# Kernel tuning notes

Hardware: AMD Instinct MI355X
Metric: run time of the kernel (lower is better)

The kernel has to match this reference:

```python
import jax, jax.numpy as jnp
import numpy as np

N_NODES = 50000


def _gcn_conv(x, edge_index, W, b, n_nodes):
    # PyG GCNConv: add self loops, symmetric normalization, then
    # out[dst] = sum_{src->dst} norm * (x[src] @ W) + b
    src, dst = edge_index[0], edge_index[1]
    loop = jnp.arange(n_nodes, dtype=src.dtype)
    src = jnp.concatenate([src, loop])
    dst = jnp.concatenate([dst, loop])
    deg = jax.ops.segment_sum(jnp.ones_like(src, dtype=x.dtype), dst, num_segments=n_nodes)
    dinv = jnp.where(deg > 0, jax.lax.rsqrt(deg), 0.0)
    norm = dinv[src] * dinv[dst]                      # [E+N]
    h = x @ W                                         # [N, out] dense GEMM first (in >= out here)
    msg = h[src] * norm[:, None]                      # gather + scale
    out = jax.ops.segment_sum(msg, dst, num_segments=n_nodes)  # scatter-add
    return out + b


def setup_inputs() -> dict:
    key = jax.random.key(0)
    k = jax.random.split(key, 5)
    in_c, hid_c, out_c = 128, 128, 64
    n, e = N_NODES, 800000
    x = jax.random.normal(k[0], (n, in_c), dtype=jnp.float32)
    edge_index = jax.random.randint(k[1], (2, e), 0, n, dtype=jnp.int64)
    # Glorot-ish scaled weights
    W1 = jax.random.normal(k[2], (in_c, hid_c), dtype=jnp.float32) * (1.0 / np.sqrt(in_c))
    b1 = jnp.zeros((hid_c,), dtype=jnp.float32)
    W2 = jax.random.normal(k[3], (hid_c, out_c), dtype=jnp.float32) * (1.0 / np.sqrt(hid_c))
    b2 = jnp.zeros((out_c,), dtype=jnp.float32)
    return {"x": x, "edge_index": edge_index, "W1": W1, "b1": b1, "W2": W2, "b2": b2}


def reference(x, edge_index, W1, b1, W2, b2):
    # Net.encode: conv1 -> relu -> conv2
    h = _gcn_conv(x, edge_index, W1, b1, N_NODES)
    h = jax.nn.relu(h)
    z = _gcn_conv(h, edge_index, W2, b2, N_NODES)
    return z
```

## Files before the change

kernel.cpp:

```cpp
#include <hip/hip_runtime.h>
#include <math.h>

constexpr int C_IN  = 128;
constexpr int C_HID = 128;
constexpr int C_OUT = 64;

typedef short bf8   __attribute__((ext_vector_type(8)));
typedef float f32x4 __attribute__((ext_vector_type(4)));

__device__ __forceinline__ int wave_incl_scan(int v, int lane) {
    #pragma unroll
    for (int off = 1; off < 64; off <<= 1) {
        int u = __shfl_up(v, off, 64);
        if (lane >= off) v += u;
    }
    return v;
}
__device__ __forceinline__ short b16(float f) {
    unsigned int u = __float_as_uint(f);
    u += 0x7FFFu + ((u >> 16) & 1u);
    return (short)(u >> 16);
}
__device__ __forceinline__ unsigned int bpack(float a, float b) {
    unsigned int ua = __float_as_uint(a), ub = __float_as_uint(b);
    ua += 0x7FFFu + ((ua >> 16) & 1u);
    ub += 0x7FFFu + ((ub >> 16) & 1u);
    return (ua >> 16) | (ub & 0xFFFF0000u);
}
__device__ __forceinline__ void acc8(float* a, const uint4 v) {
    a[0] += __uint_as_float(v.x << 16);
    a[1] += __uint_as_float(v.x & 0xFFFF0000u);
    a[2] += __uint_as_float(v.y << 16);
    a[3] += __uint_as_float(v.y & 0xFFFF0000u);
    a[4] += __uint_as_float(v.z << 16);
    a[5] += __uint_as_float(v.z & 0xFFFF0000u);
    a[6] += __uint_as_float(v.w << 16);
    a[7] += __uint_as_float(v.w & 0xFFFF0000u);
}

__global__ __launch_bounds__(256) void k_zero(int* __restrict__ p, int n4) {
    int i = blockIdx.x * 256 + threadIdx.x;
    if (i < n4) reinterpret_cast<int4*>(p)[i] = make_int4(0, 0, 0, 0);
}

__global__ __launch_bounds__(256) void k_count2(const int* __restrict__ dst, int e,
                                                int* __restrict__ cnt,
                                                int* __restrict__ slot) {
    int i = blockIdx.x * 256 + threadIdx.x;
    int base = i * 4;
    if (base >= e) return;
    if (base + 3 < e) {
        int4 d4 = *reinterpret_cast<const int4*>(dst + base);
        int4 s4;
        s4.x = atomicAdd(&cnt[d4.x], 1);
        s4.y = atomicAdd(&cnt[d4.y], 1);
        s4.z = atomicAdd(&cnt[d4.z], 1);
        s4.w = atomicAdd(&cnt[d4.w], 1);
        *reinterpret_cast<int4*>(slot + base) = s4;
    } else {
        for (int q = base; q < e; ++q) slot[q] = atomicAdd(&cnt[dst[q]], 1);
    }
}

__global__ __launch_bounds__(256) void k_scanAB(const int* __restrict__ cnt, int n,
                                                int* __restrict__ rowstart,
                                                int* __restrict__ blocksum,
                                                int* __restrict__ blockoff,
                                                int* __restrict__ ticket,
                                                float* __restrict__ dinv) {
    __shared__ int swave[4];
    __shared__ int amLast;
    const int tid = threadIdx.x, lane = tid & 63, w = tid >> 6;
    const int idx = blockIdx.x * 1024 + tid * 4;
    int4 c = make_int4(0, 0, 0, 0);
    if (idx + 3 < n) {
        c = *reinterpret_cast<const int4*>(cnt + idx);
    } else if (idx < n) {
        c.x = cnt[idx];
        if (idx + 1 < n) c.y = cnt[idx + 1];
        if (idx + 2 < n) c.z = cnt[idx + 2];
        if (idx + 3 < n) c.w = cnt[idx + 3];
    }
    if (idx + 0 < n) dinv[idx + 0] = rsqrtf((float)(c.x + 1));
    if (idx + 1 < n) dinv[idx + 1] = rsqrtf((float)(c.y + 1));
    if (idx + 2 < n) dinv[idx + 2] = rsqrtf((float)(c.z + 1));
    if (idx + 3 < n) dinv[idx + 3] = rsqrtf((float)(c.w + 1));

    const int s4 = c.x + c.y + c.z + c.w;
    const int incl = wave_incl_scan(s4, lane);
    if (lane == 63) swave[w] = incl;
    __syncthreads();
    int base = incl - s4;
    #pragma unroll
    for (int j = 0; j < 4; ++j) if (j < w) base += swave[j];

    if (idx + 3 < n) {
        int4 o;
        o.x = base;
        o.y = base + c.x;
        o.z = base + c.x + c.y;
        o.w = base + c.x + c.y + c.z;
        *reinterpret_cast<int4*>(rowstart + idx) = o;
    } else if (idx < n) {
        int acc = base;
        rowstart[idx] = acc; acc += c.x;
        if (idx + 1 < n) { rowstart[idx + 1] = acc; acc += c.y; }
        if (idx + 2 < n) { rowstart[idx + 2] = acc; acc += c.z; }
        if (idx + 3 < n) { rowstart[idx + 3] = acc; }
    }

    if (tid == 0) {
        int tot = swave[0] + swave[1] + swave[2] + swave[3];
        blocksum[blockIdx.x] = tot;
        if (blockIdx.x == gridDim.x - 1) rowstart[n] = tot;
        __threadfence();
        amLast = (atomicAdd(ticket, 1) == (int)gridDim.x - 1);
    }
    __syncthreads();
    if (amLast && tid < 64) {
        __threadfence();
        volatile int* bs = blocksum;
        const int nb = gridDim.x;
        int v = (tid < nb) ? bs[tid] : 0;
        int incl2 = wave_incl_scan(v, tid);
        if (tid < nb) blockoff[tid] = incl2 - v;
    }
}

__global__ __launch_bounds__(256) void k_fillgemm1(
    const int* __restrict__ src, const int* __restrict__ dst,
    const int* __restrict__ slot, int e, int nfb,
    const int* __restrict__ rowstart, const int* __restrict__ blockoff,
    unsigned short* __restrict__ nbr,
    const float* __restrict__ x, const float* __restrict__ W,
    const float* __restrict__ dinv, unsigned short* __restrict__ h1b, int n) {
    __shared__ short wf[8 * 4 * 64 * 8];
    if (blockIdx.x < nfb) {
        int i = blockIdx.x * 256 + threadIdx.x;
        int base = i * 4;
        if (base >= e) return;
        if (base + 3 < e) {
            int4 d4 = *reinterpret_cast<const int4*>(dst + base);
            int4 s4 = *reinterpret_cast<const int4*>(src + base);
            int4 t4 = *reinterpret_cast<const int4*>(slot + base);
            nbr[rowstart[d4.x] + blockoff[d4.x >> 10] + t4.x] = (unsigned short)s4.x;
            nbr[rowstart[d4.y] + blockoff[d4.y >> 10] + t4.y] = (unsigned short)s4.y;
            nbr[rowstart[d4.z] + blockoff[d4.z >> 10] + t4.z] = (unsigned short)s4.z;
            nbr[rowstart[d4.w] + blockoff[d4.w >> 10] + t4.w] = (unsigned short)s4.w;
        } else {
            for (int q = base; q < e; ++q) {
                int d = dst[q];
                nbr[rowstart[d] + blockoff[d >> 10] + slot[q]] = (unsigned short)src[q];
            }
        }
        return;
    }
    const int tid = threadIdx.x;
    for (int i = tid; i < 2048; i += 256) {
        const int l = i & 63, kt = (i >> 6) & 3, ct = i >> 8;
        const int krow = kt * 32 + ((l >> 4) << 3);
        const int col  = ct * 16 + (l & 15);
        const float* wp = W + (size_t)krow * C_HID + col;
        uint4 u;
        u.x = bpack(wp[0 * C_HID], wp[1 * C_HID]);
        u.y = bpack(wp[2 * C_HID], wp[3 * C_HID]);
        u.z = bpack(wp[4 * C_HID], wp[5 * C_HID]);
        u.w = bpack(wp[6 * C_HID], wp[7 * C_HID]);
        reinterpret_cast<uint4*>(wf)[i] = u;
    }
    __syncthreads();

    const int l = tid & 63, w = tid >> 6;
    const int row0 = (blockIdx.x - nfb) * 64 + w * 16;
    int arow = row0 + (l & 15);
    if (arow >= n) arow = n - 1;
    const float* xr = x + (size_t)arow * C_IN + ((l >> 4) << 3);

    bf8 a[4];
    #pragma unroll
    for (int kt = 0; kt < 4; ++kt) {
        float4 p0 = *reinterpret_cast<const float4*>(xr + kt * 32);
        float4 p1 = *reinterpret_cast<const float4*>(xr + kt * 32 + 4);
        bf8 t;
        t[0] = b16(p0.x); t[1] = b16(p0.y); t[2] = b16(p0.z); t[3] = b16(p0.w);
        t[4] = b16(p1.x); t[5] = b16(p1.y); t[6] = b16(p1.z); t[7] = b16(p1.w);
        a[kt] = t;
    }

    f32x4 acc[8];
    #pragma unroll
    for (int ct = 0; ct < 8; ++ct) acc[ct] = (f32x4){0.f, 0.f, 0.f, 0.f};
    const bf8* bw = reinterpret_cast<const bf8*>(wf);
    #pragma unroll
    for (int kt = 0; kt < 4; ++kt)
        #pragma unroll
        for (int ct = 0; ct < 8; ++ct)
            acc[ct] = __builtin_amdgcn_mfma_f32_16x16x32_bf16(
                a[kt], bw[(ct * 4 + kt) * 64 + l], acc[ct], 0, 0, 0);

    const int rbase = row0 + ((l >> 4) << 2);
    float dv[4];
    #pragma unroll
    for (int r = 0; r < 4; ++r) {
        int rr = rbase + r;
        dv[r] = (rr < n) ? dinv[rr] : 0.f;
    }
    #pragma unroll
    for (int ct = 0; ct < 8; ++ct) {
        const int col = ct * 16 + (l & 15);
        #pragma unroll
        for (int r = 0; r < 4; ++r) {
            int rr = rbase + r;
            if (rr < n)
                h1b[(size_t)rr * C_HID + col] = (unsigned short)b16(acc[ct][r] * dv[r]);
        }
    }
}

__global__ __launch_bounds__(256) void k_agg1gemm2(
    const uint4* __restrict__ h1v,
    const int* __restrict__ rowstart, const int* __restrict__ blockoff,
    const unsigned short* __restrict__ nbr,
    const float* __restrict__ dinv, const float* __restrict__ b1,
    const float* __restrict__ W2,
    unsigned short* __restrict__ h2b, int n) {
    __shared__ short wf[4 * 4 * 64 * 8];
    __shared__ uint4 actl[64 * 16];
    const int tid  = threadIdx.x;
    const int row0 = blockIdx.x * 64;

    for (int i = tid; i < 1024; i += 256) {
        const int l = i & 63, kt = (i >> 6) & 3, ct = i >> 8;
        const int krow = kt * 32 + ((l >> 4) << 3);
        const int col  = ct * 16 + (l & 15);
        const float* wp = W2 + (size_t)krow * C_OUT + col;
        uint4 u;
        u.x = bpack(wp[0 * C_OUT], wp[1 * C_OUT]);
        u.y = bpack(wp[2 * C_OUT], wp[3 * C_OUT]);
        u.z = bpack(wp[4 * C_OUT], wp[5 * C_OUT]);
        u.w = bpack(wp[6 * C_OUT], wp[7 * C_OUT]);
        reinterpret_cast<uint4*>(wf)[i] = u;
    }

    const int c8 = tid & 15, grp = tid >> 4;
    const float4 bb0 = reinterpret_cast<const float4*>(b1)[2 * c8 + 0];
    const float4 bb1 = reinterpret_cast<const float4*>(b1)[2 * c8 + 1];
    #pragma unroll
    for (int it = 0; it < 4; ++it) {
        const int r    = grp + 16 * it;
        const int node = row0 + r;
        uint4 p = make_uint4(0, 0, 0, 0);
        if (node < n) {
            float a8[8] = {0.f, 0.f, 0.f, 0.f, 0.f, 0.f, 0.f, 0.f};
            acc8(a8, h1v[(size_t)node * 16 + c8]);
            int j   = rowstart[node]     + blockoff[node >> 10];
            int end = rowstart[node + 1] + blockoff[(node + 1) >> 10];
            for (; j + 1 < end; j += 2) {
                int s0 = nbr[j], s1 = nbr[j + 1];
                uint4 v0 = h1v[(size_t)s0 * 16 + c8];
                uint4 v1 = h1v[(size_t)s1 * 16 + c8];
                acc8(a8, v0); acc8(a8, v1);
            }
            if (j < end) acc8(a8, h1v[(size_t)nbr[j] * 16 + c8]);
            const float sc = dinv[node];
            p.x = bpack(fmaxf(sc * a8[0] + bb0.x, 0.f), fmaxf(sc * a8[1] + bb0.y, 0.f));
            p.y = bpack(fmaxf(sc * a8[2] + bb0.z, 0.f), fmaxf(sc * a8[3] + bb0.w, 0.f));
            p.z = bpack(fmaxf(sc * a8[4] + bb1.x, 0.f), fmaxf(sc * a8[5] + bb1.y, 0.f));
            p.w = bpack(fmaxf(sc * a8[6] + bb1.z, 0.f), fmaxf(sc * a8[7] + bb1.w, 0.f));
        }
        actl[r * 16 + (c8 ^ (r & 15))] = p;
    }
    __syncthreads();

    const int l = tid & 63, w = tid >> 6;
    bf8 a[4];
    #pragma unroll
    for (int kt = 0; kt < 4; ++kt) {
        const int row   = w * 16 + (l & 15);
        const int chunk = kt * 4 + (l >> 4);
        uint4 v = actl[row * 16 + (chunk ^ (row & 15))];
        a[kt] = *reinterpret_cast<bf8*>(&v);
    }

    f32x4 acc[4];
    #pragma unroll
    for (int ct = 0; ct < 4; ++ct) acc[ct] = (f32x4){0.f, 0.f, 0.f, 0.f};
    const bf8* bw = reinterpret_cast<const bf8*>(wf);
    #pragma unroll
    for (int kt = 0; kt < 4; ++kt)
        #pragma unroll
        for (int ct = 0; ct < 4; ++ct)
            acc[ct] = __builtin_amdgcn_mfma_f32_16x16x32_bf16(
                a[kt], bw[(ct * 4 + kt) * 64 + l], acc[ct], 0, 0, 0);

    const int rbase = row0 + w * 16 + ((l >> 4) << 2);
    float dv[4];
    #pragma unroll
    for (int r = 0; r < 4; ++r) {
        int rr = rbase + r;
        dv[r] = (rr < n) ? dinv[rr] : 0.f;
    }
    #pragma unroll
    for (int ct = 0; ct < 4; ++ct) {
        const int col = ct * 16 + (l & 15);
        #pragma unroll
        for (int r = 0; r < 4; ++r) {
            int rr = rbase + r;
            if (rr < n)
                h2b[(size_t)rr * C_OUT + col] = (unsigned short)b16(acc[ct][r] * dv[r]);
        }
    }
}

__global__ __launch_bounds__(256) void k_agg2b(const uint4* __restrict__ h2v,
                                               const int* __restrict__ rowstart,
                                               const int* __restrict__ blockoff,
                                               const unsigned short* __restrict__ nbr,
                                               const float* __restrict__ dinv,
                                               const float* __restrict__ b2,
                                               float* __restrict__ outb, int n) {
    int node = blockIdx.x * 32 + (threadIdx.x >> 3);
    if (node >= n) return;
    const int lane8 = threadIdx.x & 7;
    float a8[8] = {0.f, 0.f, 0.f, 0.f, 0.f, 0.f, 0.f, 0.f};
    acc8(a8, h2v[(size_t)node * 8 + lane8]);
    int j   = rowstart[node]     + blockoff[node >> 10];
    int end = rowstart[node + 1] + blockoff[(node + 1) >> 10];
    for (; j + 1 < end; j += 2) {
        int s0 = nbr[j], s1 = nbr[j + 1];
        uint4 v0 = h2v[(size_t)s0 * 8 + lane8];
        uint4 v1 = h2v[(size_t)s1 * 8 + lane8];
        acc8(a8, v0); acc8(a8, v1);
    }
    if (j < end) acc8(a8, h2v[(size_t)nbr[j] * 8 + lane8]);
    const float s = dinv[node];
    const float4 c0 = reinterpret_cast<const float4*>(b2)[2 * lane8 + 0];
    const float4 c1 = reinterpret_cast<const float4*>(b2)[2 * lane8 + 1];
    float4 o0, o1;
    o0.x = s * a8[0] + c0.x; o0.y = s * a8[1] + c0.y;
    o0.z = s * a8[2] + c0.z; o0.w = s * a8[3] + c0.w;
    o1.x = s * a8[4] + c1.x; o1.y = s * a8[5] + c1.y;
    o1.z = s * a8[6] + c1.z; o1.w = s * a8[7] + c1.w;
    reinterpret_cast<float4*>(outb)[node * 16 + 2 * lane8 + 0] = o0;
    reinterpret_cast<float4*>(outb)[node * 16 + 2 * lane8 + 1] = o1;
}

extern "C" void kernel_launch(void* const* d_in, const int* in_sizes, int n_in,
                              void* d_out, int out_size, void* d_ws, size_t ws_size,
                              hipStream_t stream) {
    const float* x  = (const float*)d_in[0];
    const int*   ei = (const int*)d_in[1];
    const float* W1 = (const float*)d_in[2];
    const float* b1 = (const float*)d_in[3];
    const float* W2 = (const float*)d_in[4];
    const float* b2 = (const float*)d_in[5];

    const int n = in_sizes[0] / C_IN;
    const int e = in_sizes[1] / 2;
    const int* src = ei;
    const int* dst = ei + e;

    char* ws = (char*)d_ws;
    float* dinv     = (float*)(ws);
    int*   cnt      = (int*)  (ws + (1u << 18));
    int*   rowstart = (int*)  (ws + (2u << 18));
    int*   blocksum = (int*)  (ws + (3u << 18));
    int*   blockoff = (int*)  (ws + (3u << 18) + 4096);
    int*   slot     = (int*)  (ws + (1u << 20));
    unsigned short* nbr = (unsigned short*)(ws + (5u << 20));
    unsigned short* h1b = (unsigned short*)(ws + (8u << 20));
    unsigned short* h2b = (unsigned short*)(ws + (21u << 20));
    int*   ticket   = cnt + n;
    float* outb     = (float*)d_out;

    const int NB  = (n + 1023) / 1024;
    const int nz4 = (n + 1 + 3) / 4;
    const int nFB = ((e + 3) / 4 + 255) / 256;
    const int nGB = (n + 63) / 64;

    k_zero     <<<(nz4 + 255) / 256, 256, 0, stream>>>(cnt, nz4);
    k_count2   <<<nFB, 256, 0, stream>>>(dst, e, cnt, slot);
    k_scanAB   <<<NB, 256, 0, stream>>>(cnt, n, rowstart, blocksum, blockoff, ticket, dinv);
    k_fillgemm1<<<nFB + nGB, 256, 0, stream>>>(src, dst, slot, e, nFB, rowstart, blockoff,
                                               nbr, x, W1, dinv, h1b, n);
    k_agg1gemm2<<<nGB, 256, 0, stream>>>((const uint4*)h1b, rowstart, blockoff, nbr,
                                         dinv, b1, W2, h2b, n);
    k_agg2b    <<<(n + 31) / 32, 256, 0, stream>>>((const uint4*)h2b, rowstart, blockoff, nbr,
                                                   dinv, b2, outb, n);
}
```

Before: 142.9 us.

## Split fused layer-1 aggregation and layer-2 GEMM into two kernels

The fused aggregate-then-GEMM kernel is split in two. One kernel gathers neighbours with 16 nodes per block and writes the bf16 post-ReLU activations to a global buffer. A separate MFMA GEMM kernel then reads them from global memory instead of LDS. The aim is better load balance and occupancy for the irregular gather by removing the 64-row block barrier and the shared staging. The cost is an extra global write and read of the activations (about 12.8 MB), plus one more kernel launch.

```diff
diff --git a/kernel.cpp b/kernel.cpp
--- a/kernel.cpp
+++ b/kernel.cpp
@@ -217,17 +217,46 @@
     }
 }
 
-__global__ __launch_bounds__(256) void k_agg1gemm2(
-    const uint4* __restrict__ h1v,
-    const int* __restrict__ rowstart, const int* __restrict__ blockoff,
-    const unsigned short* __restrict__ nbr,
-    const float* __restrict__ dinv, const float* __restrict__ b1,
-    const float* __restrict__ W2,
-    unsigned short* __restrict__ h2b, int n) {
+__global__ __launch_bounds__(256) void k_agg1b16(const uint4* __restrict__ h1v,
+                                                 const int* __restrict__ rowstart,
+                                                 const int* __restrict__ blockoff,
+                                                 const unsigned short* __restrict__ nbr,
+                                                 const float* __restrict__ dinv,
+                                                 const float* __restrict__ b1,
+                                                 uint4* __restrict__ actb,
+                                                 int n) {
+    int node = blockIdx.x * 16 + (threadIdx.x >> 4);
+    if (node >= n) return;
+    const int c8 = threadIdx.x & 15;
+    float a8[8] = {0.f, 0.f, 0.f, 0.f, 0.f, 0.f, 0.f, 0.f};
+    acc8(a8, h1v[(size_t)node * 16 + c8]);
+    int j   = rowstart[node]     + blockoff[node >> 10];
+    int end = rowstart[node + 1] + blockoff[(node + 1) >> 10];
+    for (; j + 1 < end; j += 2) {
+        int s0 = nbr[j], s1 = nbr[j + 1];
+        uint4 v0 = h1v[(size_t)s0 * 16 + c8];
+        uint4 v1 = h1v[(size_t)s1 * 16 + c8];
+        acc8(a8, v0); acc8(a8, v1);
+    }
+    if (j < end) acc8(a8, h1v[(size_t)nbr[j] * 16 + c8]);
+    const float sc = dinv[node];
+    const float4 bb0 = reinterpret_cast<const float4*>(b1)[2 * c8 + 0];
+    const float4 bb1 = reinterpret_cast<const float4*>(b1)[2 * c8 + 1];
+    uint4 p;
+    p.x = bpack(fmaxf(sc * a8[0] + bb0.x, 0.f), fmaxf(sc * a8[1] + bb0.y, 0.f));
+    p.y = bpack(fmaxf(sc * a8[2] + bb0.z, 0.f), fmaxf(sc * a8[3] + bb0.w, 0.f));
+    p.z = bpack(fmaxf(sc * a8[4] + bb1.x, 0.f), fmaxf(sc * a8[5] + bb1.y, 0.f));
+    p.w = bpack(fmaxf(sc * a8[6] + bb1.z, 0.f), fmaxf(sc * a8[7] + bb1.w, 0.f));
+    actb[(size_t)node * 16 + c8] = p;
+}
+
+__global__ __launch_bounds__(256) void k_gemm2m(const unsigned short* __restrict__ actb,
+                                                const float* __restrict__ W2,
+                                                const float* __restrict__ dinv,
+                                                unsigned short* __restrict__ h2b,
+                                                int n) {
     __shared__ short wf[4 * 4 * 64 * 8];
-    __shared__ uint4 actl[64 * 16];
-    const int tid  = threadIdx.x;
-    const int row0 = blockIdx.x * 64;
+    const int tid = threadIdx.x;
 
     for (int i = tid; i < 1024; i += 256) {
         const int l = i & 63, kt = (i >> 6) & 3, ct = i >> 8;
@@ -241,46 +270,18 @@
         u.w = bpack(wp[6 * C_OUT], wp[7 * C_OUT]);
         reinterpret_cast<uint4*>(wf)[i] = u;
     }
-
-    const int c8 = tid & 15, grp = tid >> 4;
-    const float4 bb0 = reinterpret_cast<const float4*>(b1)[2 * c8 + 0];
-    const float4 bb1 = reinterpret_cast<const float4*>(b1)[2 * c8 + 1];
-    #pragma unroll
-    for (int it = 0; it < 4; ++it) {
-        const int r    = grp + 16 * it;
-        const int node = row0 + r;
-        uint4 p = make_uint4(0, 0, 0, 0);
-        if (node < n) {
-            float a8[8] = {0.f, 0.f, 0.f, 0.f, 0.f, 0.f, 0.f, 0.f};
-            acc8(a8, h1v[(size_t)node * 16 + c8]);
-            int j   = rowstart[node]     + blockoff[node >> 10];
-            int end = rowstart[node + 1] + blockoff[(node + 1) >> 10];
-            for (; j + 1 < end; j += 2) {
-                int s0 = nbr[j], s1 = nbr[j + 1];
-                uint4 v0 = h1v[(size_t)s0 * 16 + c8];
-                uint4 v1 = h1v[(size_t)s1 * 16 + c8];
-                acc8(a8, v0); acc8(a8, v1);
-            }
-            if (j < end) acc8(a8, h1v[(size_t)nbr[j] * 16 + c8]);
-            const float sc = dinv[node];
-            p.x = bpack(fmaxf(sc * a8[0] + bb0.x, 0.f), fmaxf(sc * a8[1] + bb0.y, 0.f));
-            p.y = bpack(fmaxf(sc * a8[2] + bb0.z, 0.f), fmaxf(sc * a8[3] + bb0.w, 0.f));
-            p.z = bpack(fmaxf(sc * a8[4] + bb1.x, 0.f), fmaxf(sc * a8[5] + bb1.y, 0.f));
-            p.w = bpack(fmaxf(sc * a8[6] + bb1.z, 0.f), fmaxf(sc * a8[7] + bb1.w, 0.f));
-        }
-        actl[r * 16 + (c8 ^ (r & 15))] = p;
-    }
     __syncthreads();
 
     const int l = tid & 63, w = tid >> 6;
+    const int row0 = blockIdx.x * 64 + w * 16;
+    int arow = row0 + (l & 15);
+    if (arow >= n) arow = n - 1;
+    const unsigned short* ar = actb + (size_t)arow * C_HID + ((l >> 4) << 3);
+
     bf8 a[4];
     #pragma unroll
-    for (int kt = 0; kt < 4; ++kt) {
-        const int row   = w * 16 + (l & 15);
-        const int chunk = kt * 4 + (l >> 4);
-        uint4 v = actl[row * 16 + (chunk ^ (row & 15))];
-        a[kt] = *reinterpret_cast<bf8*>(&v);
-    }
+    for (int kt = 0; kt < 4; ++kt)
+        a[kt] = *reinterpret_cast<const bf8*>(ar + kt * 32);
 
     f32x4 acc[4];
     #pragma unroll
@@ -293,7 +294,7 @@
             acc[ct] = __builtin_amdgcn_mfma_f32_16x16x32_bf16(
                 a[kt], bw[(ct * 4 + kt) * 64 + l], acc[ct], 0, 0, 0);
 
-    const int rbase = row0 + w * 16 + ((l >> 4) << 2);
+    const int rbase = row0 + ((l >> 4) << 2);
     float dv[4];
     #pragma unroll
     for (int r = 0; r < 4; ++r) {
@@ -367,9 +368,10 @@
     int*   blocksum = (int*)  (ws + (3u << 18));
     int*   blockoff = (int*)  (ws + (3u << 18) + 4096);
     int*   slot     = (int*)  (ws + (1u << 20));
-    unsigned short* nbr = (unsigned short*)(ws + (5u << 20));
-    unsigned short* h1b = (unsigned short*)(ws + (8u << 20));
-    unsigned short* h2b = (unsigned short*)(ws + (21u << 20));
+    unsigned short* nbr  = (unsigned short*)(ws + (5u << 20));
+    unsigned short* h1b  = (unsigned short*)(ws + (8u << 20));
+    unsigned short* actb = (unsigned short*)(ws + (21u << 20));
+    unsigned short* h2b  = (unsigned short*)(ws + (34u << 20));
     int*   ticket   = cnt + n;
     float* outb     = (float*)d_out;
 
@@ -383,8 +385,9 @@
     k_scanAB   <<<NB, 256, 0, stream>>>(cnt, n, rowstart, blocksum, blockoff, ticket, dinv);
     k_fillgemm1<<<nFB + nGB, 256, 0, stream>>>(src, dst, slot, e, nFB, rowstart, blockoff,
                                                nbr, x, W1, dinv, h1b, n);
-    k_agg1gemm2<<<nGB, 256, 0, stream>>>((const uint4*)h1b, rowstart, blockoff, nbr,
-                                         dinv, b1, W2, h2b, n);
+    k_agg1b16  <<<(n + 15) / 16, 256, 0, stream>>>((const uint4*)h1b, rowstart, blockoff, nbr,
+                                                   dinv, b1, (uint4*)actb, n);
+    k_gemm2m   <<<nGB, 256, 0, stream>>>(actb, W2, dinv, h2b, n);
     k_agg2b    <<<(n + 31) / 32, 256, 0, stream>>>((const uint4*)h2b, rowstart, blockoff, nbr,
                                                    dinv, b2, outb, n);
 }
```

After: 135.3 us. -5.3%, faster.

## Make layer-1 aggregation wave-local with 8 lanes per node and 16 channels each

Applied to the files above, without the earlier changes.

The fused aggregate+GEMM2 kernel now gives each wave its own 16 nodes and stages them in a per-wave LDS tile, which removes the block-wide barrier between aggregation and the MFMA GEMM. Each node is now handled by 8 lanes that each load two 16-byte chunks per neighbor, rather than 16 lanes loading one chunk each. This doubles per-lane memory-level parallelism and accumulator registers. The LDS XOR swizzle is dropped, which may introduce bank conflicts when the MFMA operands are read.

```diff
diff --git a/kernel.cpp b/kernel.cpp
--- a/kernel.cpp
+++ b/kernel.cpp
@@ -217,7 +217,7 @@
     }
 }
 
-__global__ __launch_bounds__(256) void k_agg1gemm2(
+__global__ __launch_bounds__(256) void k_aggmm2(
     const uint4* __restrict__ h1v,
     const int* __restrict__ rowstart, const int* __restrict__ blockoff,
     const unsigned short* __restrict__ nbr,
@@ -225,9 +225,8 @@
     const float* __restrict__ W2,
     unsigned short* __restrict__ h2b, int n) {
     __shared__ short wf[4 * 4 * 64 * 8];
-    __shared__ uint4 actl[64 * 16];
-    const int tid  = threadIdx.x;
-    const int row0 = blockIdx.x * 64;
+    __shared__ uint4 actl[4][16][16];
+    const int tid = threadIdx.x;
 
     for (int i = tid; i < 1024; i += 256) {
         const int l = i & 63, kt = (i >> 6) & 3, ct = i >> 8;
@@ -241,47 +240,64 @@
         u.w = bpack(wp[6 * C_OUT], wp[7 * C_OUT]);
         reinterpret_cast<uint4*>(wf)[i] = u;
     }
-
-    const int c8 = tid & 15, grp = tid >> 4;
-    const float4 bb0 = reinterpret_cast<const float4*>(b1)[2 * c8 + 0];
-    const float4 bb1 = reinterpret_cast<const float4*>(b1)[2 * c8 + 1];
-    #pragma unroll
-    for (int it = 0; it < 4; ++it) {
-        const int r    = grp + 16 * it;
-        const int node = row0 + r;
-        uint4 p = make_uint4(0, 0, 0, 0);
+    __syncthreads();
+
+    const int l = tid & 63, wid = tid >> 6;
+    const int u = blockIdx.x * 4 + wid;
+    const int node0 = u * 16;
+    if (node0 >= n) return;
+    const float4* b1f4 = reinterpret_cast<const float4*>(b1);
+
+    const int p2 = l & 7;
+    #pragma unroll
+    for (int t = 0; t < 2; ++t) {
+        const int g    = t * 8 + (l >> 3);
+        const int node = node0 + g;
+        uint4 pk0 = make_uint4(0, 0, 0, 0), pk1 = make_uint4(0, 0, 0, 0);
         if (node < n) {
-            float a8[8] = {0.f, 0.f, 0.f, 0.f, 0.f, 0.f, 0.f, 0.f};
-            acc8(a8, h1v[(size_t)node * 16 + c8]);
+            float a16[16];
+            #pragma unroll
+            for (int q = 0; q < 16; ++q) a16[q] = 0.f;
+            const uint4* self = h1v + (size_t)node * 16 + p2;
+            acc8(a16 + 0, self[0]);
+            acc8(a16 + 8, self[8]);
             int j   = rowstart[node]     + blockoff[node >> 10];
             int end = rowstart[node + 1] + blockoff[(node + 1) >> 10];
             for (; j + 1 < end; j += 2) {
                 int s0 = nbr[j], s1 = nbr[j + 1];
-                uint4 v0 = h1v[(size_t)s0 * 16 + c8];
-                uint4 v1 = h1v[(size_t)s1 * 16 + c8];
-                acc8(a8, v0); acc8(a8, v1);
+                const uint4* r0 = h1v + (size_t)s0 * 16 + p2;
+                const uint4* r1 = h1v + (size_t)s1 * 16 + p2;
+                uint4 v00 = r0[0], v01 = r0[8];
+                uint4 v10 = r1[0], v11 = r1[8];
+                acc8(a16 + 0, v00); acc8(a16 + 8, v01);
+                acc8(a16 + 0, v10); acc8(a16 + 8, v11);
             }
-            if (j < end) acc8(a8, h1v[(size_t)nbr[j] * 16 + c8]);
+            if (j < end) {
+                const uint4* r0 = h1v + (size_t)nbr[j] * 16 + p2;
+                acc8(a16 + 0, r0[0]); acc8(a16 + 8, r0[8]);
+            }
             const float sc = dinv[node];
-            p.x = bpack(fmaxf(sc * a8[0] + bb0.x, 0.f), fmaxf(sc * a8[1] + bb0.y, 0.f));
-            p.y = bpack(fmaxf(sc * a8[2] + bb0.z, 0.f), fmaxf(sc * a8[3] + bb0.w, 0.f));
-            p.z = bpack(fmaxf(sc * a8[4] + bb1.x, 0.f), fmaxf(sc * a8[5] + bb1.y, 0.f));
-            p.w = bpack(fmaxf(sc * a8[6] + bb1.z, 0.f), fmaxf(sc * a8[7] + bb1.w, 0.f));
+            float4 ba = b1f4[2 * p2 + 0],  bbv = b1f4[2 * p2 + 1];
+            pk0.x = bpack(fmaxf(sc * a16[0] + ba.x, 0.f),  fmaxf(sc * a16[1] + ba.y, 0.f));
+            pk0.y = bpack(fmaxf(sc * a16[2] + ba.z, 0.f),  fmaxf(sc * a16[3] + ba.w, 0.f));
+            pk0.z = bpack(fmaxf(sc * a16[4] + bbv.x, 0.f), fmaxf(sc * a16[5] + bbv.y, 0.f));
+            pk0.w = bpack(fmaxf(sc * a16[6] + bbv.z, 0.f), fmaxf(sc * a16[7] + bbv.w, 0.f));
+            float4 bc = b1f4[2 * (p2 + 8) + 0], bd = b1f4[2 * (p2 + 8) + 1];
+            pk1.x = bpack(fmaxf(sc * a16[8]  + bc.x, 0.f), fmaxf(sc * a16[9]  + bc.y, 0.f));
+            pk1.y = bpack(fmaxf(sc * a16[10] + bc.z, 0.f), fmaxf(sc * a16[11] + bc.w, 0.f));
+            pk1.z = bpack(fmaxf(sc * a16[12] + bd.x, 0.f), fmaxf(sc * a16[13] + bd.y, 0.f));
+            pk1.w = bpack(fmaxf(sc * a16[14] + bd.z, 0.f), fmaxf(sc * a16[15] + bd.w, 0.f));
         }
-        actl[r * 16 + (c8 ^ (r & 15))] = p;
-    }
-    __syncthreads();
-
-    const int l = tid & 63, w = tid >> 6;
+        actl[wid][g][p2]     = pk0;
+        actl[wid][g][p2 + 8] = pk1;
+    }
+
     bf8 a[4];
     #pragma unroll
     for (int kt = 0; kt < 4; ++kt) {
-        const int row   = w * 16 + (l & 15);
-        const int chunk = kt * 4 + (l >> 4);
-        uint4 v = actl[row * 16 + (chunk ^ (row & 15))];
-        a[kt] = *reinterpret_cast<bf8*>(&v);
-    }
-
+        uint4 av = actl[wid][l & 15][kt * 4 + (l >> 4)];
+        a[kt] = *reinterpret_cast<bf8*>(&av);
+    }
     f32x4 acc[4];
     #pragma unroll
     for (int ct = 0; ct < 4; ++ct) acc[ct] = (f32x4){0.f, 0.f, 0.f, 0.f};
@@ -293,7 +309,7 @@
             acc[ct] = __builtin_amdgcn_mfma_f32_16x16x32_bf16(
                 a[kt], bw[(ct * 4 + kt) * 64 + l], acc[ct], 0, 0, 0);
 
-    const int rbase = row0 + w * 16 + ((l >> 4) << 2);
+    const int rbase = node0 + ((l >> 4) << 2);
     float dv[4];
     #pragma unroll
     for (int r = 0; r < 4; ++r) {
@@ -377,13 +393,15 @@
     const int nz4 = (n + 1 + 3) / 4;
     const int nFB = ((e + 3) / 4 + 255) / 256;
     const int nGB = (n + 63) / 64;
+    const int nU  = (n + 15) / 16;
+    const int nAB = (nU + 3) / 4;
 
     k_zero     <<<(nz4 + 255) / 256, 256, 0, stream>>>(cnt, nz4);
     k_count2   <<<nFB, 256, 0, stream>>>(dst, e, cnt, slot);
     k_scanAB   <<<NB, 256, 0, stream>>>(cnt, n, rowstart, blocksum, blockoff, ticket, dinv);
     k_fillgemm1<<<nFB + nGB, 256, 0, stream>>>(src, dst, slot, e, nFB, rowstart, blockoff,
                                                nbr, x, W1, dinv, h1b, n);
-    k_agg1gemm2<<<nGB, 256, 0, stream>>>((const uint4*)h1b, rowstart, blockoff, nbr,
+    k_aggmm2   <<<nAB, 256, 0, stream>>>((const uint4*)h1b, rowstart, blockoff, nbr,
                                          dinv, b1, W2, h2b, n);
     k_agg2b    <<<(n + 31) / 32, 256, 0, stream>>>((const uint4*)h2b, rowstart, blockoff, nbr,
                                                    dinv, b2, outb, n);
```

Measured after the change: 132.3 us, median of 2. 7.4% less time.
